# Performance work log

Hardware: AMD Instinct MI355X
Metric: run time of the kernel (lower is better)

The kernel has to match this reference:

```python
import jax, jax.numpy as jnp
import numpy as np

B, S, D, E, H, K = 2, 2048, 1024, 8, 4096, 2


def setup_inputs() -> dict:
    key = jax.random.key(0)
    ks = jax.random.split(key, 7)
    sd = 1.0 / np.sqrt(D)
    sh = 1.0 / np.sqrt(H)
    return {
        "x": jax.random.normal(ks[0], (B, S, D), dtype=jnp.float32),
        "router_w": jax.random.uniform(ks[1], (D, E), jnp.float32, -sd, sd),
        "router_b": jnp.zeros((E,), jnp.float32),
        "w1": jax.random.uniform(ks[2], (E, D, H), jnp.float32, -sd, sd),
        "b1": jnp.zeros((E, H), jnp.float32),
        "w2": jax.random.uniform(ks[3], (E, H, D), jnp.float32, -sh, sh),
        "b2": jnp.zeros((E, D), jnp.float32),
    }


def reference(x, router_w, router_b, w1, b1, w2, b2):
    # Router: softmax over experts, then top-k and renormalize
    router_logits = jnp.einsum("bsd,de->bse", x, router_w) + router_b
    router_probs = jax.nn.softmax(router_logits, axis=-1)
    top_k_probs, top_k_indices = jax.lax.top_k(router_probs, K)  # [B,S,K]
    top_k_probs = top_k_probs / jnp.sum(top_k_probs, axis=-1, keepdims=True)

    # Dense all-expert FFN (Block assumed: Linear -> GELU -> Linear)
    h = jax.nn.gelu(jnp.einsum("bsd,edh->bseh", x, w1) + b1)  # [B,S,E,H]
    expert_outputs = jnp.einsum("bseh,ehd->bsed", h, w2) + b2  # [B,S,E,D]

    # Gather top-k experts per token and combine with renormalized probs
    idx = top_k_indices[..., None]  # [B,S,K,1]
    selected = jnp.take_along_axis(expert_outputs, idx, axis=2)  # [B,S,K,D]
    return jnp.sum(selected * top_k_probs[..., None], axis=2)  # [B,S,D]
```

## Files before the change

kernel.cpp:

```cpp
#include <hip/hip_runtime.h>
#include <hip/hip_bf16.h>

#define TOK   4096
#define DDIM  1024
#define NEXP  8
#define HDIM  4096
#define KSEL  2
#define NPAIR (TOK * KSEL)
#define NSPLIT 2
#define MAXT  72

typedef __attribute__((ext_vector_type(8))) _Float16 f16x8;
typedef __attribute__((ext_vector_type(4))) _Float16 f16x4;
typedef __attribute__((ext_vector_type(4))) float    f32x4;

__device__ __forceinline__ void gload16(const void* g, void* l) {
  __builtin_amdgcn_global_load_lds((const __attribute__((address_space(1))) void*)g,
                                   (__attribute__((address_space(3))) void*)l, 16, 0, 0);
}

__device__ __forceinline__ float gelu_tanh(float u) {
  float inner = 0.7978845608028654f * (u + 0.044715f * u * u * u);
  float t2 = __expf(2.f * inner);
  return u - u / (t2 + 1.f);
}

__global__ __launch_bounds__(256) void k_prep(const float* __restrict__ x,
    const float* __restrict__ rw, const float* __restrict__ rb,
    const float* __restrict__ w1, const float* __restrict__ w2,
    int* __restrict__ tidx, float* __restrict__ tw, _Float16* __restrict__ xb,
    _Float16* __restrict__ w1t, _Float16* __restrict__ w2t) {
  if (blockIdx.x < 1024) {
    const int t    = blockIdx.x * 4 + (threadIdx.x >> 6);
    const int lane = threadIdx.x & 63;
    const float* xr = x + (size_t)t * DDIM;
    _Float16*   xbr = xb + (size_t)t * DDIM;
    float acc[NEXP];
#pragma unroll
    for (int e = 0; e < NEXP; ++e) acc[e] = 0.f;
    for (int d0 = lane * 4; d0 < DDIM; d0 += 256) {
      const float4 xv = *(const float4*)(xr + d0);
      f16x4 hx;
      hx[0] = (_Float16)xv.x; hx[1] = (_Float16)xv.y;
      hx[2] = (_Float16)xv.z; hx[3] = (_Float16)xv.w;
      *(f16x4*)(xbr + d0) = hx;
#pragma unroll
      for (int i = 0; i < 4; ++i) {
        const float xs = (&xv.x)[i];
        const float4 r0 = *(const float4*)(rw + (size_t)(d0 + i) * NEXP);
        const float4 r1 = *(const float4*)(rw + (size_t)(d0 + i) * NEXP + 4);
        acc[0] += xs * r0.x; acc[1] += xs * r0.y; acc[2] += xs * r0.z; acc[3] += xs * r0.w;
        acc[4] += xs * r1.x; acc[5] += xs * r1.y; acc[6] += xs * r1.z; acc[7] += xs * r1.w;
      }
    }
#pragma unroll
    for (int e = 0; e < NEXP; ++e) {
      float v = acc[e];
#pragma unroll
      for (int s = 32; s; s >>= 1) v += __shfl_xor(v, s, 64);
      acc[e] = v;
    }
    if (lane == 0) {
      float lg[NEXP];
#pragma unroll
      for (int e = 0; e < NEXP; ++e) lg[e] = acc[e] + rb[e];
      int i0 = 0;
#pragma unroll
      for (int e = 1; e < NEXP; ++e) if (lg[e] > lg[i0]) i0 = e;
      int i1 = -1; float best = -3.4e38f;
#pragma unroll
      for (int e = 0; e < NEXP; ++e) {
        if (e == i0) continue;
        if (lg[e] > best) { best = lg[e]; i1 = e; }
      }
      float w0 = 1.f / (1.f + expf(lg[i1] - lg[i0]));
      tidx[t * 2]     = i0;  tidx[t * 2 + 1] = i1;
      tw[t * 2]       = w0;  tw[t * 2 + 1]   = 1.f - w0;
    }
    return;
  }
  __shared__ _Float16 tile[64][66];
  const int bx = blockIdx.x - 1024;
  const int zz = bx >> 10;
  const int xx = bx & 1023;
  const float* ip; _Float16* op; int Rr, Cc, i0, j0;
  if (zz < NEXP) {
    ip = w1 + (size_t)zz * DDIM * HDIM;  op = w1t + (size_t)zz * DDIM * HDIM;
    Rr = DDIM; Cc = HDIM;
    i0 = (xx >> 6) * 64; j0 = (xx & 63) * 64;
  } else {
    ip = w2 + (size_t)(zz - NEXP) * HDIM * DDIM;  op = w2t + (size_t)(zz - NEXP) * HDIM * DDIM;
    Rr = HDIM; Cc = DDIM;
    i0 = (xx >> 4) * 64; j0 = (xx & 15) * 64;
  }
  const int tx = threadIdx.x & 15, ty = threadIdx.x >> 4;
#pragma unroll
  for (int rr = 0; rr < 4; ++rr) {
    int r = ty + rr * 16;
    float4 v = *(const float4*)(ip + (size_t)(i0 + r) * Cc + j0 + tx * 4);
    tile[r][tx * 4 + 0] = (_Float16)v.x;
    tile[r][tx * 4 + 1] = (_Float16)v.y;
    tile[r][tx * 4 + 2] = (_Float16)v.z;
    tile[r][tx * 4 + 3] = (_Float16)v.w;
  }
  __syncthreads();
  {
    const int c  = threadIdx.x >> 2;
    const int s0 = (threadIdx.x & 3) * 16;
    f16x8 v0, v1;
#pragma unroll
    for (int k = 0; k < 8; ++k) { v0[k] = tile[s0 + k][c]; v1[k] = tile[s0 + 8 + k][c]; }
    _Float16* outp = op + (size_t)(j0 + c) * Rr + i0 + s0;
    *(f16x8*)outp       = v0;
    *(f16x8*)(outp + 8) = v1;
  }
}

__global__ __launch_bounds__(1024) void k_scan(const int* __restrict__ tidx,
                       const float* __restrict__ tw,
                       int* __restrict__ offs,
                       int* __restrict__ row_token, float* __restrict__ row_w,
                       int* __restrict__ inv,
                       int* __restrict__ tlist, int* __restrict__ tcount) {
  __shared__ int hist[NEXP];
  __shared__ int soff[NEXP + 1];
  __shared__ int scur[NEXP];
  if (threadIdx.x < NEXP) hist[threadIdx.x] = 0;
  __syncthreads();
  const int lane = threadIdx.x & 63;
  int e_loc[NPAIR / 1024];
#pragma unroll
  for (int it = 0; it < NPAIR / 1024; ++it) {
    const int p = it * 1024 + threadIdx.x;
    const int e = tidx[p];
    e_loc[it] = e;
#pragma unroll
    for (int ee = 0; ee < NEXP; ++ee) {
      unsigned long long m = __ballot(e == ee);
      if (m && lane == 0) atomicAdd(&hist[ee], __popcll(m));
    }
  }
  __syncthreads();
  if (threadIdx.x == 0) {
    int run = 0;
    for (int e = 0; e < NEXP; ++e) { soff[e] = run; scur[e] = run; run += hist[e]; }
    soff[NEXP] = run;
    for (int e = 0; e <= NEXP; ++e) offs[e] = soff[e];
    int cnt = 0;
    for (int e = 0; e < NEXP; ++e) {
      const int ne = soff[e + 1] - soff[e];
      for (int m = 0; m < ne; m += 128) tlist[cnt++] = (e << 8) | (m >> 7);
    }
    *tcount = cnt;
  }
  __syncthreads();
#pragma unroll
  for (int it = 0; it < NPAIR / 1024; ++it) {
    const int p = it * 1024 + threadIdx.x;
    const int e = e_loc[it];
    int pos = 0;
#pragma unroll
    for (int ee = 0; ee < NEXP; ++ee) {
      unsigned long long m = __ballot(e == ee);
      if (!m) continue;
      int base = 0;
      if (lane == 0) base = atomicAdd(&scur[ee], __popcll(m));
      base = __shfl(base, 0, 64);
      if (e == ee) pos = base + __popcll(m & ((1ull << lane) - 1ull));
    }
    row_token[pos] = p >> 1;
    row_w[pos]     = tw[p];
    inv[p]         = pos;
  }
}

#define BM 128
#define BN 128
#define BKK 32


__global__ __launch_bounds__(256) void k_gemm1(
    const _Float16* __restrict__ xb,
    const _Float16* __restrict__ w1t,
    const float* __restrict__ b1,
    const int* __restrict__ offs,
    const int* __restrict__ row_token,
    const int* __restrict__ tlist, const int* __restrict__ tcount,
    _Float16* __restrict__ hbuf) {
  const int bid = blockIdx.x;
  const int t   = bid >> 5;
  if (t >= *tcount) return;
  const int tl  = tlist[t];
  const int e   = tl >> 8;
  const int m0  = (tl & 255) * BM;
  const int n0  = (bid & 31) * BN;
  const int off0 = offs[e];
  const int ne   = offs[e + 1] - off0;
  const int mrem = ne - m0;

  __shared__ __align__(16) char smem[32768];

  const int tid = threadIdx.x;
  const int wv = tid >> 6, lane = tid & 63;
  const int l15 = lane & 15;
  const int wr = wv >> 1, wc = wv & 1;

  const int rA0 = (wv * 2 + 0) * 16 + (lane >> 2);
  const int rA1 = (wv * 2 + 1) * 16 + (lane >> 2);
  const char* a_c = (const char*)xb;
  const char* b_c = (const char*)(w1t + (size_t)e * HDIM * DDIM);
  const int rc0 = (rA0 < mrem) ? rA0 : (mrem - 1);
  const int rc1 = (rA1 < mrem) ? rA1 : (mrem - 1);
  const char* ap0 = a_c + (size_t)row_token[off0 + m0 + rc0] * (DDIM * 2)
                        + (((lane & 3) ^ ((rA0 >> 1) & 3)) << 4);
  const char* ap1 = a_c + (size_t)row_token[off0 + m0 + rc1] * (DDIM * 2)
                        + (((lane & 3) ^ ((rA1 >> 1) & 3)) << 4);
  const char* bp0 = b_c + (size_t)(n0 + rA0) * (DDIM * 2)
                        + (((lane & 3) ^ ((rA0 >> 1) & 3)) << 4);
  const char* bp1 = b_c + (size_t)(n0 + rA1) * (DDIM * 2)
                        + (((lane & 3) ^ ((rA1 >> 1) & 3)) << 4);
  char* ldsA0 = smem + (wv * 2 + 0) * 1024;
  char* ldsA1 = smem + (wv * 2 + 1) * 1024;
  char* ldsB0 = smem + 16384 + (wv * 2 + 0) * 1024;
  char* ldsB1 = smem + 16384 + (wv * 2 + 1) * 1024;

  const unsigned foff = (unsigned)(((lane >> 4) ^ ((l15 >> 1) & 3)) << 4);

  f32x4 acc[4][4] = {};
  const int NT = DDIM / BKK;

  gload16(ap0, ldsA0); gload16(ap1, ldsA1);
  gload16(bp0, ldsB0); gload16(bp1, ldsB1);

#pragma unroll 2
  for (int ks = 0; ks < NT; ++ks) {
    const int cur = ks & 1;
    if (ks + 1 < NT) {
      const int nb = (cur ^ 1) * 8192;
      const size_t kb = (size_t)(ks + 1) * 64;
      gload16(ap0 + kb, ldsA0 + nb); gload16(ap1 + kb, ldsA1 + nb);
      gload16(bp0 + kb, ldsB0 + nb); gload16(bp1 + kb, ldsB1 + nb);
      asm volatile("s_waitcnt vmcnt(4)" ::: "memory");
    } else {
      asm volatile("s_waitcnt vmcnt(0)" ::: "memory");
    }
    __builtin_amdgcn_sched_barrier(0);
    __builtin_amdgcn_s_barrier();
    const char* Ab = smem + cur * 8192;
    const char* Bb = smem + 16384 + cur * 8192;
    f16x8 af[4], bfr[4];
#pragma unroll
    for (int m = 0; m < 4; ++m)
      af[m] = *(const f16x8*)(Ab + (wr * 64 + m * 16 + l15) * 64 + foff);
#pragma unroll
    for (int n = 0; n < 4; ++n)
      bfr[n] = *(const f16x8*)(Bb + (wc * 64 + n * 16 + l15) * 64 + foff);
#pragma unroll
    for (int m = 0; m < 4; ++m)
#pragma unroll
      for (int n = 0; n < 4; ++n)
        acc[m][n] = __builtin_amdgcn_mfma_f32_16x16x32_f16(af[m], bfr[n], acc[m][n], 0, 0, 0);
    __builtin_amdgcn_sched_barrier(0);
    __builtin_amdgcn_s_barrier();
  }

  float bias[4];
#pragma unroll
  for (int n = 0; n < 4; ++n)
    bias[n] = b1[(size_t)e * HDIM + n0 + wc * 64 + n * 16 + l15];
#pragma unroll
  for (int m = 0; m < 4; ++m) {
#pragma unroll
    for (int j = 0; j < 4; ++j) {
      int row = wr * 64 + m * 16 + (lane >> 4) * 4 + j;
#pragma unroll
      for (int n = 0; n < 4; ++n) {
        int col = wc * 64 + n * 16 + l15;
        *(_Float16*)(smem + (row << 8) + (((col << 1) ^ ((row & 15) << 4)))) =
            (_Float16)gelu_tanh(acc[m][n][j] + bias[n]);
      }
    }
  }
  __syncthreads();
  {
    const int srow = tid >> 1, half = tid & 1;
    if (srow < mrem) {
      _Float16* hr = hbuf + (size_t)(off0 + m0 + srow) * HDIM + n0 + half * 64;
#pragma unroll
      for (int i = 0; i < 8; ++i) {
        f16x8 v = *(const f16x8*)(smem + (srow << 8) + (((half * 128 + i * 16) ^ ((srow & 15) << 4))));
        *(f16x8*)(hr + i * 8) = v;
      }
    }
  }
}

__global__ __launch_bounds__(256) void k_gemm2(
    const _Float16* __restrict__ hbuf,
    const _Float16* __restrict__ w2t,
    const int* __restrict__ offs,
    const int* __restrict__ tlist, const int* __restrict__ tcount,
    _Float16* __restrict__ yb) {
  const int bid = blockIdx.x;
  const int t   = bid >> 4;
  if (t >= *tcount) return;
  const int tl  = tlist[t];
  const int e   = tl >> 8;
  const int m0  = (tl & 255) * BM;
  const int sub = bid & 15;
  const int kh  = sub >> 3;
  const int n0  = (sub & 7) * BN;
  const int off0 = offs[e];
  const int ne   = offs[e + 1] - off0;
  const int mrem = ne - m0;

  __shared__ __align__(16) char smem[32768];

  const int tid = threadIdx.x;
  const int wv = tid >> 6, lane = tid & 63;
  const int l15 = lane & 15;
  const int wr = wv >> 1, wc = wv & 1;

  const int rA0 = (wv * 2 + 0) * 16 + (lane >> 2);
  const int rA1 = (wv * 2 + 1) * 16 + (lane >> 2);
  const char* a_c = (const char*)hbuf;
  const char* b_c = (const char*)(w2t + (size_t)e * DDIM * HDIM);
  const int rc0 = (rA0 < mrem) ? rA0 : (mrem - 1);
  const int rc1 = (rA1 < mrem) ? rA1 : (mrem - 1);
  const size_t khb = (size_t)kh * ((HDIM / NSPLIT) * 2);
  const char* ap0 = a_c + (size_t)(off0 + m0 + rc0) * (HDIM * 2) + khb
                        + (((lane & 3) ^ ((rA0 >> 1) & 3)) << 4);
  const char* ap1 = a_c + (size_t)(off0 + m0 + rc1) * (HDIM * 2) + khb
                        + (((lane & 3) ^ ((rA1 >> 1) & 3)) << 4);
  const char* bp0 = b_c + (size_t)(n0 + rA0) * (HDIM * 2) + khb
                        + (((lane & 3) ^ ((rA0 >> 1) & 3)) << 4);
  const char* bp1 = b_c + (size_t)(n0 + rA1) * (HDIM * 2) + khb
                        + (((lane & 3) ^ ((rA1 >> 1) & 3)) << 4);
  char* ldsA0 = smem + (wv * 2 + 0) * 1024;
  char* ldsA1 = smem + (wv * 2 + 1) * 1024;
  char* ldsB0 = smem + 16384 + (wv * 2 + 0) * 1024;
  char* ldsB1 = smem + 16384 + (wv * 2 + 1) * 1024;

  const unsigned foff = (unsigned)(((lane >> 4) ^ ((l15 >> 1) & 3)) << 4);

  f32x4 acc[4][4] = {};
  const int NT = (HDIM / NSPLIT) / BKK;

  gload16(ap0, ldsA0); gload16(ap1, ldsA1);
  gload16(bp0, ldsB0); gload16(bp1, ldsB1);

#pragma unroll 2
  for (int ks = 0; ks < NT; ++ks) {
    const int cur = ks & 1;
    if (ks + 1 < NT) {
      const int nb = (cur ^ 1) * 8192;
      const size_t kb = (size_t)(ks + 1) * 64;
      gload16(ap0 + kb, ldsA0 + nb); gload16(ap1 + kb, ldsA1 + nb);
      gload16(bp0 + kb, ldsB0 + nb); gload16(bp1 + kb, ldsB1 + nb);
      asm volatile("s_waitcnt vmcnt(4)" ::: "memory");
    } else {
      asm volatile("s_waitcnt vmcnt(0)" ::: "memory");
    }
    __builtin_amdgcn_sched_barrier(0);
    __builtin_amdgcn_s_barrier();
    const char* Ab = smem + cur * 8192;
    const char* Bb = smem + 16384 + cur * 8192;
    f16x8 af[4], bfr[4];
#pragma unroll
    for (int m = 0; m < 4; ++m)
      af[m] = *(const f16x8*)(Ab + (wr * 64 + m * 16 + l15) * 64 + foff);
#pragma unroll
    for (int n = 0; n < 4; ++n)
      bfr[n] = *(const f16x8*)(Bb + (wc * 64 + n * 16 + l15) * 64 + foff);
#pragma unroll
    for (int m = 0; m < 4; ++m)
#pragma unroll
      for (int n = 0; n < 4; ++n)
        acc[m][n] = __builtin_amdgcn_mfma_f32_16x16x32_f16(af[m], bfr[n], acc[m][n], 0, 0, 0);
    __builtin_amdgcn_sched_barrier(0);
    __builtin_amdgcn_s_barrier();
  }

  _Float16* ypart = yb + (size_t)kh * NPAIR * DDIM;
#pragma unroll
  for (int m = 0; m < 4; ++m) {
#pragma unroll
    for (int j = 0; j < 4; ++j) {
      int row = wr * 64 + m * 16 + (lane >> 4) * 4 + j;
#pragma unroll
      for (int n = 0; n < 4; ++n) {
        int col = wc * 64 + n * 16 + l15;
        *(_Float16*)(smem + (row << 8) + (((col << 1) ^ ((row & 15) << 4)))) =
            (_Float16)acc[m][n][j];
      }
    }
  }
  __syncthreads();
  {
    const int srow = tid >> 1, half = tid & 1;
    if (srow < mrem) {
      _Float16* yr = ypart + (size_t)(off0 + m0 + srow) * DDIM + n0 + half * 64;
#pragma unroll
      for (int i = 0; i < 8; ++i) {
        f16x8 v = *(const f16x8*)(smem + (srow << 8) + (((half * 128 + i * 16) ^ ((srow & 15) << 4))));
        *(f16x8*)(yr + i * 8) = v;
      }
    }
  }
}

__global__ __launch_bounds__(256) void k_combine(const _Float16* __restrict__ yb,
    const int* __restrict__ inv, const int* __restrict__ tidx,
    const float* __restrict__ tw, const float* __restrict__ b2,
    float* __restrict__ out) {
  const int t  = blockIdx.x * 2 + (threadIdx.x >> 7);
  const int c8 = (threadIdx.x & 127) * 8;
  const int g0 = inv[2 * t],  g1 = inv[2 * t + 1];
  const int e0 = tidx[2 * t], e1 = tidx[2 * t + 1];
  const float w0 = tw[2 * t], w1 = tw[2 * t + 1];
  const _Float16* y1p = yb + (size_t)NPAIR * DDIM;
  f16x8 a0 = *(const f16x8*)(yb  + (size_t)g0 * DDIM + c8);
  f16x8 a1 = *(const f16x8*)(y1p + (size_t)g0 * DDIM + c8);
  f16x8 b0 = *(const f16x8*)(yb  + (size_t)g1 * DDIM + c8);
  f16x8 b1v = *(const f16x8*)(y1p + (size_t)g1 * DDIM + c8);
  float o[8];
#pragma unroll
  for (int i = 0; i < 8; ++i) {
    float bA = b2[(size_t)e0 * DDIM + c8 + i];
    float bB = b2[(size_t)e1 * DDIM + c8 + i];
    o[i] = w0 * ((float)a0[i] + (float)a1[i] + bA) + w1 * ((float)b0[i] + (float)b1v[i] + bB);
  }
  float* op = out + (size_t)t * DDIM + c8;
  *(float4*)op       = make_float4(o[0], o[1], o[2], o[3]);
  *(float4*)(op + 4) = make_float4(o[4], o[5], o[6], o[7]);
}

extern "C" void kernel_launch(void* const* d_in, const int* in_sizes, int n_in,
                              void* d_out, int out_size, void* d_ws, size_t ws_size,
                              hipStream_t stream) {
  const float* x  = (const float*)d_in[0];
  const float* rw = (const float*)d_in[1];
  const float* rb = (const float*)d_in[2];
  const float* w1 = (const float*)d_in[3];
  const float* b1 = (const float*)d_in[4];
  const float* w2 = (const float*)d_in[5];
  const float* b2 = (const float*)d_in[6];
  float* out = (float*)d_out;
  char* ws = (char*)d_ws;

  int*      tidx    = (int*)(ws + 0);
  float*    tw      = (float*)(ws + 32768);
  int*      tcount  = (int*)(ws + 65536);
  int*      tlist   = (int*)(ws + 65544);
  int*      offs    = (int*)(ws + 65856);
  int*      row_tok = (int*)(ws + 66048);
  float*    row_w   = (float*)(ws + 98816);
  int*      inv     = (int*)(ws + 131584);
  _Float16* xb      = (_Float16*)(ws + 164352);
  _Float16* wtA     = (_Float16*)(ws + 8552960);
  _Float16* wtB     = (_Float16*)(ws + 75661824);
  _Float16* hb      = (_Float16*)(ws + 142770688);
  _Float16* yb      = wtA;

  k_prep<<<dim3(1024 + 16 * 1024), 256, 0, stream>>>(x, rw, rb, w1, w2,
                                                     tidx, tw, xb, wtA, wtB);
  k_scan<<<dim3(1), 1024, 0, stream>>>(tidx, tw, offs, row_tok, row_w, inv, tlist, tcount);
  k_gemm1<<<dim3(MAXT * 32), 256, 0, stream>>>(xb, wtA, b1, offs, row_tok, tlist, tcount, hb);
  k_gemm2<<<dim3(MAXT * 16), 256, 0, stream>>>(hb, wtB, offs, tlist, tcount, yb);
  k_combine<<<dim3(TOK / 2), 256, 0, stream>>>(yb, inv, tidx, tw, b2, out);
}
```

Measured before the change: 346.1 us.

## Load B operand fragments directly from global into registers, bypassing LDS

Both expert GEMM kernels now fetch the weight (B) fragments straight from global memory into double-buffered registers instead of staging them through LDS with global_load_lds. This removes the LDS writes and reads for B and frees half the shared memory. The cost is that each wave pair sharing a column tile loads B redundantly (wr=0 and wr=1 both fetch it), so global and L2 traffic for weights doubles. It also uses uncoalesced 16-byte-per-lane loads spread across rows, and the vmcnt wait count was changed by hand, which risks mis-ordering with the indexing of the register buffer under unroll 2.

```diff
diff --git a/kernel.cpp b/kernel.cpp
--- a/kernel.cpp
+++ b/kernel.cpp
@@ -202,7 +202,7 @@
 
   const int tid = threadIdx.x;
   const int wv = tid >> 6, lane = tid & 63;
-  const int l15 = lane & 15;
+  const int l15 = lane & 15, l16 = lane >> 4;
   const int wr = wv >> 1, wc = wv & 1;
 
   const int rA0 = (wv * 2 + 0) * 16 + (lane >> 2);
@@ -215,22 +215,21 @@
                         + (((lane & 3) ^ ((rA0 >> 1) & 3)) << 4);
   const char* ap1 = a_c + (size_t)row_token[off0 + m0 + rc1] * (DDIM * 2)
                         + (((lane & 3) ^ ((rA1 >> 1) & 3)) << 4);
-  const char* bp0 = b_c + (size_t)(n0 + rA0) * (DDIM * 2)
-                        + (((lane & 3) ^ ((rA0 >> 1) & 3)) << 4);
-  const char* bp1 = b_c + (size_t)(n0 + rA1) * (DDIM * 2)
-                        + (((lane & 3) ^ ((rA1 >> 1) & 3)) << 4);
   char* ldsA0 = smem + (wv * 2 + 0) * 1024;
   char* ldsA1 = smem + (wv * 2 + 1) * 1024;
-  char* ldsB0 = smem + 16384 + (wv * 2 + 0) * 1024;
-  char* ldsB1 = smem + 16384 + (wv * 2 + 1) * 1024;
+
+  const char* bB = b_c + (size_t)(n0 + wc * 64 + l15) * (DDIM * 2) + l16 * 16;
 
   const unsigned foff = (unsigned)(((lane >> 4) ^ ((l15 >> 1) & 3)) << 4);
 
   f32x4 acc[4][4] = {};
+  f16x8 bn[2][4];
   const int NT = DDIM / BKK;
 
   gload16(ap0, ldsA0); gload16(ap1, ldsA1);
-  gload16(bp0, ldsB0); gload16(bp1, ldsB1);
+#pragma unroll
+  for (int n = 0; n < 4; ++n)
+    bn[0][n] = *(const f16x8*)(bB + n * (16 * DDIM * 2));
 
 #pragma unroll 2
   for (int ks = 0; ks < NT; ++ks) {
@@ -239,27 +238,25 @@
       const int nb = (cur ^ 1) * 8192;
       const size_t kb = (size_t)(ks + 1) * 64;
       gload16(ap0 + kb, ldsA0 + nb); gload16(ap1 + kb, ldsA1 + nb);
-      gload16(bp0 + kb, ldsB0 + nb); gload16(bp1 + kb, ldsB1 + nb);
-      asm volatile("s_waitcnt vmcnt(4)" ::: "memory");
+#pragma unroll
+      for (int n = 0; n < 4; ++n)
+        bn[cur ^ 1][n] = *(const f16x8*)(bB + n * (16 * DDIM * 2) + kb);
+      asm volatile("s_waitcnt vmcnt(6)" ::: "memory");
     } else {
       asm volatile("s_waitcnt vmcnt(0)" ::: "memory");
     }
     __builtin_amdgcn_sched_barrier(0);
     __builtin_amdgcn_s_barrier();
     const char* Ab = smem + cur * 8192;
-    const char* Bb = smem + 16384 + cur * 8192;
-    f16x8 af[4], bfr[4];
+    f16x8 af[4];
 #pragma unroll
     for (int m = 0; m < 4; ++m)
       af[m] = *(const f16x8*)(Ab + (wr * 64 + m * 16 + l15) * 64 + foff);
 #pragma unroll
-    for (int n = 0; n < 4; ++n)
-      bfr[n] = *(const f16x8*)(Bb + (wc * 64 + n * 16 + l15) * 64 + foff);
-#pragma unroll
     for (int m = 0; m < 4; ++m)
 #pragma unroll
       for (int n = 0; n < 4; ++n)
-        acc[m][n] = __builtin_amdgcn_mfma_f32_16x16x32_f16(af[m], bfr[n], acc[m][n], 0, 0, 0);
+        acc[m][n] = __builtin_amdgcn_mfma_f32_16x16x32_f16(af[m], bn[cur][n], acc[m][n], 0, 0, 0);
     __builtin_amdgcn_sched_barrier(0);
     __builtin_amdgcn_s_barrier();
   }
@@ -318,7 +315,7 @@
 
   const int tid = threadIdx.x;
   const int wv = tid >> 6, lane = tid & 63;
-  const int l15 = lane & 15;
+  const int l15 = lane & 15, l16 = lane >> 4;
   const int wr = wv >> 1, wc = wv & 1;
 
   const int rA0 = (wv * 2 + 0) * 16 + (lane >> 2);
@@ -332,22 +329,21 @@
                         + (((lane & 3) ^ ((rA0 >> 1) & 3)) << 4);
   const char* ap1 = a_c + (size_t)(off0 + m0 + rc1) * (HDIM * 2) + khb
                         + (((lane & 3) ^ ((rA1 >> 1) & 3)) << 4);
-  const char* bp0 = b_c + (size_t)(n0 + rA0) * (HDIM * 2) + khb
-                        + (((lane & 3) ^ ((rA0 >> 1) & 3)) << 4);
-  const char* bp1 = b_c + (size_t)(n0 + rA1) * (HDIM * 2) + khb
-                        + (((lane & 3) ^ ((rA1 >> 1) & 3)) << 4);
   char* ldsA0 = smem + (wv * 2 + 0) * 1024;
   char* ldsA1 = smem + (wv * 2 + 1) * 1024;
-  char* ldsB0 = smem + 16384 + (wv * 2 + 0) * 1024;
-  char* ldsB1 = smem + 16384 + (wv * 2 + 1) * 1024;
+
+  const char* bB = b_c + (size_t)(n0 + wc * 64 + l15) * (HDIM * 2) + khb + l16 * 16;
 
   const unsigned foff = (unsigned)(((lane >> 4) ^ ((l15 >> 1) & 3)) << 4);
 
   f32x4 acc[4][4] = {};
+  f16x8 bn[2][4];
   const int NT = (HDIM / NSPLIT) / BKK;
 
   gload16(ap0, ldsA0); gload16(ap1, ldsA1);
-  gload16(bp0, ldsB0); gload16(bp1, ldsB1);
+#pragma unroll
+  for (int n = 0; n < 4; ++n)
+    bn[0][n] = *(const f16x8*)(bB + n * (16 * HDIM * 2));
 
 #pragma unroll 2
   for (int ks = 0; ks < NT; ++ks) {
@@ -356,27 +352,25 @@
       const int nb = (cur ^ 1) * 8192;
       const size_t kb = (size_t)(ks + 1) * 64;
       gload16(ap0 + kb, ldsA0 + nb); gload16(ap1 + kb, ldsA1 + nb);
-      gload16(bp0 + kb, ldsB0 + nb); gload16(bp1 + kb, ldsB1 + nb);
-      asm volatile("s_waitcnt vmcnt(4)" ::: "memory");
+#pragma unroll
+      for (int n = 0; n < 4; ++n)
+        bn[cur ^ 1][n] = *(const f16x8*)(bB + n * (16 * HDIM * 2) + kb);
+      asm volatile("s_waitcnt vmcnt(6)" ::: "memory");
     } else {
       asm volatile("s_waitcnt vmcnt(0)" ::: "memory");
     }
     __builtin_amdgcn_sched_barrier(0);
     __builtin_amdgcn_s_barrier();
     const char* Ab = smem + cur * 8192;
-    const char* Bb = smem + 16384 + cur * 8192;
-    f16x8 af[4], bfr[4];
+    f16x8 af[4];
 #pragma unroll
     for (int m = 0; m < 4; ++m)
       af[m] = *(const f16x8*)(Ab + (wr * 64 + m * 16 + l15) * 64 + foff);
 #pragma unroll
-    for (int n = 0; n < 4; ++n)
-      bfr[n] = *(const f16x8*)(Bb + (wc * 64 + n * 16 + l15) * 64 + foff);
-#pragma unroll
     for (int m = 0; m < 4; ++m)
 #pragma unroll
       for (int n = 0; n < 4; ++n)
-        acc[m][n] = __builtin_amdgcn_mfma_f32_16x16x32_f16(af[m], bfr[n], acc[m][n], 0, 0, 0);
+        acc[m][n] = __builtin_amdgcn_mfma_f32_16x16x32_f16(af[m], bn[cur][n], acc[m][n], 0, 0, 0);
     __builtin_amdgcn_sched_barrier(0);
     __builtin_amdgcn_s_barrier();
   }
```

New measurement: 547.7 us. +58.2%, slower.
